# Kernel optimization log

Measured on AMD Instinct MI355X. Metric: run time of the kernel, lower is better.

Reference implementation:

```python
import jax, jax.numpy as jnp
import numpy as np
import math

N_HEADS = 8
INPUT_DIM = 128
EMBED_DIM = 128
KEY_DIM = EMBED_DIM // N_HEADS  # 16, val_dim == key_dim
B = 4
N = 1024


def setup_inputs() -> dict:
    key = jax.random.key(0)
    ks = jax.random.split(key, 12)
    def unif(k, shape):
        stdv = 1.0 / math.sqrt(shape[-1])
        return jax.random.uniform(k, shape, jnp.float32, -stdv, stdv)
    return {
        "q": jax.random.normal(ks[0], (B, N, INPUT_DIM), jnp.float32),
        "out_source_attn": jax.random.normal(ks[1], (N_HEADS, B, N, N), jnp.float32),
        "st_edge": jax.random.normal(ks[2], (N_HEADS, B, N, N), jnp.float32),
        "W_query": unif(ks[3], (N_HEADS, INPUT_DIM, KEY_DIM)),
        "W_key": unif(ks[4], (N_HEADS, INPUT_DIM, KEY_DIM)),
        "W_val": unif(ks[5], (N_HEADS, INPUT_DIM, KEY_DIM)),
        "w1": unif(ks[6], (8, 16)),  # Linear(16, 8) weight
        "b1": unif(ks[7], (8,)),
        "w2": unif(ks[8], (8, 8)),   # Linear(8, 8) weight
        "b2": unif(ks[9], (8,)),
        "W_out": unif(ks[10], (N_HEADS, KEY_DIM, EMBED_DIM)),
    }


def reference(q, out_source_attn, st_edge, W_query, W_key, W_val, w1, b1, w2, b2, W_out):
    norm = 1.0 / math.sqrt(KEY_DIM)
    # per-head projections: (h, B, N, k)
    Q = jnp.einsum('bni,hik->hbnk', q, W_query)
    K = jnp.einsum('bni,hik->hbnk', q, W_key)
    V = jnp.einsum('bni,hiv->hbnv', q, W_val)
    # compatibility scores + spatio-temporal edge bias, scaled
    compat = (jnp.einsum('hbnk,hbmk->hbnm', Q, K) + st_edge) * norm
    # concat on head axis -> (16, B, N, N)
    scores = jnp.concatenate([compat, out_source_attn], axis=0)
    # tiny per-position MLP over the 16 concatenated channels
    x = scores.transpose(1, 2, 3, 0)                 # (B, N, N, 16)
    x = jax.nn.relu(x @ w1.T + b1)                   # (B, N, N, 8)
    x = x @ w2.T + b2                                # (B, N, N, 8)
    attn_logits = x.transpose(3, 0, 1, 2)            # (8, B, N, N)
    attn = jax.nn.softmax(attn_logits, axis=-1)
    heads = jnp.einsum('hbnm,hbmv->hbnv', attn, V)   # (8, B, N, v)
    out = jnp.einsum('hbnv,hve->bne', heads, W_out)  # (B, N, embed)
    return (out, out_source_attn, st_edge)
```

## Files before the change

kernel.cpp:

```cpp
#include <hip/hip_runtime.h>

typedef _Float16 half_t;
typedef _Float16 half2_t __attribute__((ext_vector_type(2)));
typedef float f4 __attribute__((ext_vector_type(4)));

#define BB 4
#define NN 1024
#define NH 8
#define KD 16
#define ID 128
#define NT 4
#define LGR 520

static constexpr size_t OUT_SZ   = (size_t)BB * NN * 128;
static constexpr size_t ATT_SZ   = (size_t)NH * BB * NN * NN;
static constexpr size_t OFF_OSS  = OUT_SZ;
static constexpr size_t OFF_ST   = OUT_SZ + ATT_SZ;
static constexpr size_t HSTRIDE  = (size_t)BB * NN * NN;

__device__ __forceinline__ float fdot2u(unsigned int a, unsigned int b, float c) {
    union { unsigned int u; half2_t h; } ua, ub;
    ua.u = a; ub.u = b;
    return __builtin_amdgcn_fdot2(ua.h, ub.h, c, false);
}

__global__ __launch_bounds__(128) void qkv_kernel(
    const float* __restrict__ q,  const float* __restrict__ Wq,
    const float* __restrict__ Wk, const float* __restrict__ Wv,
    half_t* __restrict__ Qh, half_t* __restrict__ Kp, half_t* __restrict__ Vp)
{
    const int bn = blockIdx.x;
    const int j  = threadIdx.x;
    const int h  = j >> 4, k = j & 15;
    const int b  = bn >> 10, n = bn & 1023;

    __shared__ float qrow[ID];
    qrow[j] = q[(size_t)bn * ID + j];
    __syncthreads();

    const float* wq = Wq + h * ID * KD + k;
    const float* wk = Wk + h * ID * KD + k;
    const float* wv = Wv + h * ID * KD + k;
    float aq = 0.f, ak = 0.f, av = 0.f;
#pragma unroll
    for (int i = 0; i < ID; ++i) {
        float x = qrow[i];
        aq = fmaf(x, wq[i * KD], aq);
        ak = fmaf(x, wk[i * KD], ak);
        av = fmaf(x, wv[i * KD], av);
    }
    Qh[(size_t)bn * 128 + j] = (half_t)aq;
    const size_t pr = ((size_t)((b * NH + h) * 8 + (k >> 1)) * NN + n) * 2 + (k & 1);
    Kp[pr] = (half_t)ak;
    Vp[pr] = (half_t)av;
}

__global__ __launch_bounds__(256) void vtrans_kernel(
    const unsigned int* __restrict__ Vp, half_t* __restrict__ Vt)
{
    const int bh  = blockIdx.x >> 2;
    const int nt  = blockIdx.x & 3;
    const int tid = threadIdx.x;
    const int n0  = nt * 256;

    __shared__ half_t t[16][264];

#pragma unroll
    for (int vp = 0; vp < 8; ++vp) {
        union { unsigned int u; half_t h2[2]; } c;
        c.u = Vp[((size_t)(bh * 8 + vp)) * NN + n0 + tid];
        t[2 * vp + 0][tid] = c.h2[0];
        t[2 * vp + 1][tid] = c.h2[1];
    }
    __syncthreads();
#pragma unroll
    for (int rep = 0; rep < 2; ++rep) {
        const int cch = tid + rep * 256;
        const int row = cch >> 5, col = (cch & 31) * 8;
        const uint4 vv = *reinterpret_cast<const uint4*>(&t[row][col]);
        *reinterpret_cast<uint4*>(Vt + ((size_t)(bh * 16 + row)) * NN + n0 + col) = vv;
    }
}

__global__ __launch_bounds__(512, 4) void fused_kernel(
    const float* __restrict__ oss, const float* __restrict__ st,
    const half_t* __restrict__ Qh, const unsigned int* __restrict__ Kp,
    const half_t* __restrict__ Vt,
    const float* __restrict__ w1,  const float* __restrict__ b1,
    const float* __restrict__ w2,  const float* __restrict__ b2,
    const float* __restrict__ Wout, float* __restrict__ out)
{
    const int n0  = blockIdx.x * NT;
    const int b   = blockIdx.y;
    const int tid = threadIdx.x;
    const int rg  = tid >> 7;
    const int t7  = tid & 127;
    const int mi0 = t7 * 4;

    __shared__ __align__(16) unsigned int kst[8 * 512];
    __shared__ __align__(16) half_t lg[NT * NH * LGR];
    __shared__ unsigned int qsh[NT][64];
    __shared__ float wsumPart[8][NH];
    __shared__ float headsSh[NT][128];

    if (tid < 256) qsh[tid >> 6][tid & 63] =
        reinterpret_cast<const unsigned int*>(Qh + ((size_t)(b * NN + n0 + (tid >> 6))) * 128)[tid & 63];
    if (tid < 64) wsumPart[tid >> 3][tid & 7] = 0.f;
    __syncthreads();

    const int ph   = tid >> 6;
    const int pv   = (tid >> 2) & 15;
    const int psub = tid & 3;

    float pvAcc[NT] = {0.f, 0.f, 0.f, 0.f};

#pragma unroll 1
    for (int hf = 0; hf < 2; ++hf) {
        float y[4][8];
#pragma unroll
        for (int mo = 0; mo < 4; ++mo)
#pragma unroll
            for (int o = 0; o < 8; ++o) y[mo][o] = b1[o];

#pragma unroll 1
        for (int h = 0; h < NH; ++h) {
            __syncthreads();
            {
                const int kp = tid >> 6, c = (tid & 63) * 8;
                const unsigned int* src =
                    Kp + ((size_t)((b * NH + h) * 8 + kp)) * NN + hf * 512 + c;
                const uint4 A  = *reinterpret_cast<const uint4*>(src);
                const uint4 B2 = *reinterpret_cast<const uint4*>(src + 4);
                *reinterpret_cast<uint4*>(&kst[kp * 512 + c])     = A;
                *reinterpret_cast<uint4*>(&kst[kp * 512 + c + 4]) = B2;
            }
            __syncthreads();

            const size_t idx = (size_t)h * HSTRIDE +
                ((size_t)(b * NN + n0 + rg)) * NN + hf * 512 + mi0;
            const f4 sv = __builtin_nontemporal_load(reinterpret_cast<const f4*>(st + idx));
            const f4 ov = __builtin_nontemporal_load(reinterpret_cast<const f4*>(oss + idx));
            *reinterpret_cast<f4*>(out + OFF_ST + idx)  = sv;
            *reinterpret_cast<f4*>(out + OFF_OSS + idx) = ov;
            const float svv[4] = {sv.x, sv.y, sv.z, sv.w};
            const float ovv[4] = {ov.x, ov.y, ov.z, ov.w};

            float acc[4] = {0.f, 0.f, 0.f, 0.f};
#pragma unroll
            for (int kp = 0; kp < 8; ++kp) {
                const uint4 k4 = *reinterpret_cast<const uint4*>(&kst[kp * 512 + mi0]);
                const unsigned int qp = qsh[rg][h * 8 + kp];
                acc[0] = fdot2u(k4.x, qp, acc[0]);
                acc[1] = fdot2u(k4.y, qp, acc[1]);
                acc[2] = fdot2u(k4.z, qp, acc[2]);
                acc[3] = fdot2u(k4.w, qp, acc[3]);
            }

            float w1c[8], w1o[8];
#pragma unroll
            for (int o = 0; o < 8; ++o) { w1c[o] = w1[o * 16 + h]; w1o[o] = w1[o * 16 + 8 + h]; }
#pragma unroll
            for (int mo = 0; mo < 4; ++mo) {
                const float c = (acc[mo] + svv[mo]) * 0.25f;
#pragma unroll
                for (int o = 0; o < 8; ++o)
                    y[mo][o] = fmaf(c, w1c[o], fmaf(ovv[mo], w1o[o], y[mo][o]));
            }
        }

        float lgv[8][4];
#pragma unroll
        for (int mo = 0; mo < 4; ++mo) {
            float z[8];
#pragma unroll
            for (int o = 0; o < 8; ++o) z[o] = fmaxf(y[mo][o], 0.f);
#pragma unroll
            for (int p = 0; p < 8; ++p) {
                float a = b2[p];
#pragma unroll
                for (int o = 0; o < 8; ++o) a = fmaf(z[o], w2[p * 8 + o], a);
                lgv[p][mo] = a;
            }
        }
        float psum[8];
#pragma unroll
        for (int p = 0; p < 8; ++p) {
            const float e0 = __expf(lgv[p][0]);
            const float e1 = __expf(lgv[p][1]);
            const float e2 = __expf(lgv[p][2]);
            const float e3 = __expf(lgv[p][3]);
            psum[p] = (e0 + e1) + (e2 + e3);
            union { uint2 u; half_t h4[4]; } w;
            w.h4[0] = (half_t)e0; w.h4[1] = (half_t)e1;
            w.h4[2] = (half_t)e2; w.h4[3] = (half_t)e3;
            *reinterpret_cast<uint2*>(&lg[(rg * NH + p) * LGR + mi0]) = w.u;
        }
#pragma unroll
        for (int p = 0; p < 8; ++p)
#pragma unroll
            for (int s = 32; s > 0; s >>= 1)
                psum[p] += __shfl_xor(psum[p], s);
        if ((tid & 63) == 0) {
            const int w = tid >> 6;
#pragma unroll
            for (int p = 0; p < 8; ++p) wsumPart[w][p] += psum[p];
        }
        __syncthreads();

        {
            const unsigned int* vr = reinterpret_cast<const unsigned int*>(
                Vt + ((size_t)((b * NH + ph) * KD + pv)) * NN + hf * 512);
#pragma unroll 2
            for (int c2 = 0; c2 < 16; ++c2) {
                const int mo = (c2 * 4 + psub) * 8;
                const uint4 vv = *reinterpret_cast<const uint4*>(vr + mo / 2);
#pragma unroll
                for (int r = 0; r < NT; ++r) {
                    const uint4 ww = *reinterpret_cast<const uint4*>(&lg[(r * NH + ph) * LGR + mo]);
                    pvAcc[r] = fdot2u(vv.x, ww.x, pvAcc[r]);
                    pvAcc[r] = fdot2u(vv.y, ww.y, pvAcc[r]);
                    pvAcc[r] = fdot2u(vv.z, ww.z, pvAcc[r]);
                    pvAcc[r] = fdot2u(vv.w, ww.w, pvAcc[r]);
                }
            }
        }
        __syncthreads();
    }

#pragma unroll
    for (int r = 0; r < NT; ++r) {
        pvAcc[r] += __shfl_xor(pvAcc[r], 1);
        pvAcc[r] += __shfl_xor(pvAcc[r], 2);
    }
    if (psub == 0) {
#pragma unroll
        for (int r = 0; r < NT; ++r) {
            const float s = wsumPart[2 * r][ph] + wsumPart[2 * r + 1][ph];
            headsSh[r][ph * 16 + pv] = pvAcc[r] * (1.0f / s);
        }
    }
    __syncthreads();

    {
        const int e  = tid & 127;
        const int q2 = tid >> 7;
        float a[NT] = {0.f, 0.f, 0.f, 0.f};
#pragma unroll
        for (int ii = 0; ii < 32; ++ii) {
            const int i = q2 * 32 + ii;
            const float wr = Wout[(size_t)i * 128 + e];
#pragma unroll
            for (int r = 0; r < NT; ++r) a[r] = fmaf(headsSh[r][i], wr, a[r]);
        }
        float* red = reinterpret_cast<float*>(kst);
#pragma unroll
        for (int r = 0; r < NT; ++r) red[(q2 * NT + r) * 128 + e] = a[r];
        __syncthreads();
        {
            const int r = tid >> 7, e2 = tid & 127;
            out[((size_t)(b * NN + n0 + r)) * 128 + e2] =
                red[(0 * NT + r) * 128 + e2] + red[(1 * NT + r) * 128 + e2] +
                red[(2 * NT + r) * 128 + e2] + red[(3 * NT + r) * 128 + e2];
        }
    }
}

extern "C" void kernel_launch(void* const* d_in, const int* in_sizes, int n_in,
                              void* d_out, int out_size, void* d_ws, size_t ws_size,
                              hipStream_t stream) {
    const float* q    = (const float*)d_in[0];
    const float* oss  = (const float*)d_in[1];
    const float* st   = (const float*)d_in[2];
    const float* Wq   = (const float*)d_in[3];
    const float* Wk   = (const float*)d_in[4];
    const float* Wv   = (const float*)d_in[5];
    const float* w1   = (const float*)d_in[6];
    const float* b1   = (const float*)d_in[7];
    const float* w2   = (const float*)d_in[8];
    const float* b2   = (const float*)d_in[9];
    const float* Wout = (const float*)d_in[10];
    float* out = (float*)d_out;

    half_t* Qh = (half_t*)d_ws;
    half_t* Kp = (half_t*)((char*)d_ws + 1u * 1024u * 1024u);
    half_t* Vp = (half_t*)((char*)d_ws + 2u * 1024u * 1024u);
    half_t* Vt = (half_t*)((char*)d_ws + 3u * 1024u * 1024u);

    qkv_kernel<<<dim3(BB * NN), dim3(128), 0, stream>>>(q, Wq, Wk, Wv, Qh, Kp, Vp);
    vtrans_kernel<<<dim3(32 * 4), dim3(256), 0, stream>>>((const unsigned int*)Vp, Vt);
    fused_kernel<<<dim3(NN / NT, BB), dim3(512), 0, stream>>>(
        oss, st, Qh, (const unsigned int*)Kp, Vt,
        w1, b1, w2, b2, Wout, out);
}
```

Before: 156.5 us.

## Process eight query rows per block with 256-wide key tiles

Each block now handles eight query rows instead of four, and the key dimension is split into four tiles of 256 instead of two of 512. One wavefront now owns a whole row, so the per-row softmax sum no longer needs to combine partial sums from two waves. This halves the number of blocks and doubles the reuse of each staged K tile and V row across query rows, with the goal of cutting redundant K/V traffic. The occupancy hint rises to 6 blocks per SM to go with the smaller shared-memory footprint, at the cost of twice as many tile iterations with their barriers.

```diff
diff --git a/kernel.cpp b/kernel.cpp
--- a/kernel.cpp
+++ b/kernel.cpp
@@ -9,8 +9,9 @@
 #define NH 8
 #define KD 16
 #define ID 128
-#define NT 4
-#define LGR 520
+#define NT 8
+#define QM 256
+#define LGR 264
 
 static constexpr size_t OUT_SZ   = (size_t)BB * NN * 128;
 static constexpr size_t ATT_SZ   = (size_t)NH * BB * NN * NN;
@@ -82,7 +83,7 @@
     }
 }
 
-__global__ __launch_bounds__(512, 4) void fused_kernel(
+__global__ __launch_bounds__(512, 6) void fused_kernel(
     const float* __restrict__ oss, const float* __restrict__ st,
     const half_t* __restrict__ Qh, const unsigned int* __restrict__ Kp,
     const half_t* __restrict__ Vt,
@@ -93,29 +94,29 @@
     const int n0  = blockIdx.x * NT;
     const int b   = blockIdx.y;
     const int tid = threadIdx.x;
-    const int rg  = tid >> 7;
-    const int t7  = tid & 127;
-    const int mi0 = t7 * 4;
-
-    __shared__ __align__(16) unsigned int kst[8 * 512];
+    const int rg  = tid >> 6;
+    const int t6  = tid & 63;
+    const int mi0 = t6 * 4;
+
+    __shared__ __align__(16) unsigned int kst[8 * QM];
     __shared__ __align__(16) half_t lg[NT * NH * LGR];
     __shared__ unsigned int qsh[NT][64];
-    __shared__ float wsumPart[8][NH];
+    __shared__ float wsum[NT][NH];
     __shared__ float headsSh[NT][128];
 
-    if (tid < 256) qsh[tid >> 6][tid & 63] =
-        reinterpret_cast<const unsigned int*>(Qh + ((size_t)(b * NN + n0 + (tid >> 6))) * 128)[tid & 63];
-    if (tid < 64) wsumPart[tid >> 3][tid & 7] = 0.f;
+    qsh[tid >> 6][tid & 63] = reinterpret_cast<const unsigned int*>(
+        Qh + ((size_t)(b * NN + n0 + (tid >> 6))) * 128)[tid & 63];
+    if (tid < 64) wsum[tid >> 3][tid & 7] = 0.f;
     __syncthreads();
 
     const int ph   = tid >> 6;
     const int pv   = (tid >> 2) & 15;
     const int psub = tid & 3;
 
-    float pvAcc[NT] = {0.f, 0.f, 0.f, 0.f};
+    float pvAcc[NT] = {0.f, 0.f, 0.f, 0.f, 0.f, 0.f, 0.f, 0.f};
 
 #pragma unroll 1
-    for (int hf = 0; hf < 2; ++hf) {
+    for (int qt = 0; qt < 4; ++qt) {
         float y[4][8];
 #pragma unroll
         for (int mo = 0; mo < 4; ++mo)
@@ -126,18 +127,16 @@
         for (int h = 0; h < NH; ++h) {
             __syncthreads();
             {
-                const int kp = tid >> 6, c = (tid & 63) * 8;
+                const int kp = tid >> 6, c = (tid & 63) * 4;
                 const unsigned int* src =
-                    Kp + ((size_t)((b * NH + h) * 8 + kp)) * NN + hf * 512 + c;
-                const uint4 A  = *reinterpret_cast<const uint4*>(src);
-                const uint4 B2 = *reinterpret_cast<const uint4*>(src + 4);
-                *reinterpret_cast<uint4*>(&kst[kp * 512 + c])     = A;
-                *reinterpret_cast<uint4*>(&kst[kp * 512 + c + 4]) = B2;
+                    Kp + ((size_t)((b * NH + h) * 8 + kp)) * NN + qt * QM + c;
+                *reinterpret_cast<uint4*>(&kst[kp * QM + c]) =
+                    *reinterpret_cast<const uint4*>(src);
             }
             __syncthreads();
 
             const size_t idx = (size_t)h * HSTRIDE +
-                ((size_t)(b * NN + n0 + rg)) * NN + hf * 512 + mi0;
+                ((size_t)(b * NN + n0 + rg)) * NN + qt * QM + mi0;
             const f4 sv = __builtin_nontemporal_load(reinterpret_cast<const f4*>(st + idx));
             const f4 ov = __builtin_nontemporal_load(reinterpret_cast<const f4*>(oss + idx));
             *reinterpret_cast<f4*>(out + OFF_ST + idx)  = sv;
@@ -148,7 +147,7 @@
             float acc[4] = {0.f, 0.f, 0.f, 0.f};
 #pragma unroll
             for (int kp = 0; kp < 8; ++kp) {
-                const uint4 k4 = *reinterpret_cast<const uint4*>(&kst[kp * 512 + mi0]);
+                const uint4 k4 = *reinterpret_cast<const uint4*>(&kst[kp * QM + mi0]);
                 const unsigned int qp = qsh[rg][h * 8 + kp];
                 acc[0] = fdot2u(k4.x, qp, acc[0]);
                 acc[1] = fdot2u(k4.y, qp, acc[1]);
@@ -200,18 +199,17 @@
 #pragma unroll
             for (int s = 32; s > 0; s >>= 1)
                 psum[p] += __shfl_xor(psum[p], s);
-        if ((tid & 63) == 0) {
-            const int w = tid >> 6;
-#pragma unroll
-            for (int p = 0; p < 8; ++p) wsumPart[w][p] += psum[p];
+        if (t6 == 0) {
+#pragma unroll
+            for (int p = 0; p < 8; ++p) wsum[rg][p] += psum[p];
         }
         __syncthreads();
 
         {
             const unsigned int* vr = reinterpret_cast<const unsigned int*>(
-                Vt + ((size_t)((b * NH + ph) * KD + pv)) * NN + hf * 512);
+                Vt + ((size_t)((b * NH + ph) * KD + pv)) * NN + qt * QM);
 #pragma unroll 2
-            for (int c2 = 0; c2 < 16; ++c2) {
+            for (int c2 = 0; c2 < 8; ++c2) {
                 const int mo = (c2 * 4 + psub) * 8;
                 const uint4 vv = *reinterpret_cast<const uint4*>(vr + mo / 2);
 #pragma unroll
@@ -234,17 +232,15 @@
     }
     if (psub == 0) {
 #pragma unroll
-        for (int r = 0; r < NT; ++r) {
-            const float s = wsumPart[2 * r][ph] + wsumPart[2 * r + 1][ph];
-            headsSh[r][ph * 16 + pv] = pvAcc[r] * (1.0f / s);
-        }
+        for (int r = 0; r < NT; ++r)
+            headsSh[r][ph * 16 + pv] = pvAcc[r] * (1.0f / wsum[r][ph]);
     }
     __syncthreads();
 
     {
         const int e  = tid & 127;
         const int q2 = tid >> 7;
-        float a[NT] = {0.f, 0.f, 0.f, 0.f};
+        float a[NT] = {0.f, 0.f, 0.f, 0.f, 0.f, 0.f, 0.f, 0.f};
 #pragma unroll
         for (int ii = 0; ii < 32; ++ii) {
             const int i = q2 * 32 + ii;
@@ -252,15 +248,17 @@
 #pragma unroll
             for (int r = 0; r < NT; ++r) a[r] = fmaf(headsSh[r][i], wr, a[r]);
         }
-        float* red = reinterpret_cast<float*>(kst);
+        float* red = reinterpret_cast<float*>(lg);
 #pragma unroll
         for (int r = 0; r < NT; ++r) red[(q2 * NT + r) * 128 + e] = a[r];
         __syncthreads();
-        {
-            const int r = tid >> 7, e2 = tid & 127;
+#pragma unroll
+        for (int rep = 0; rep < 2; ++rep) {
+            const int idx = rep * 512 + tid;
+            const int r = idx >> 7, e2 = idx & 127;
             out[((size_t)(b * NN + n0 + r)) * 128 + e2] =
-                red[(0 * NT + r) * 128 + e2] + red[(1 * NT + r) * 128 + e2] +
-                red[(2 * NT + r) * 128 + e2] + red[(3 * NT + r) * 128 + e2];
+                (red[(0 * NT + r) * 128 + e2] + red[(1 * NT + r) * 128 + e2]) +
+                (red[(2 * NT + r) * 128 + e2] + red[(3 * NT + r) * 128 + e2]);
         }
     }
 }
```

Result: slower. 203.4 us (+29.9%).

## Prefetch next head's K tile and edge inputs into registers across head loop

Applied to the files above, without the earlier changes.

Software-pipelines the per-head loop: the K tile and the st/oss float4 loads for head h+1 are issued into registers while head h is being computed, and the K registers are then written to shared memory at the top of the next iteration. This hides global-load latency behind the dot-product and MLP work. The launch bounds are also raised from 4 to 6 blocks per CU, which caps register use and could cause spills, especially now that the prefetch keeps more values live.

```diff
diff --git a/kernel.cpp b/kernel.cpp
--- a/kernel.cpp
+++ b/kernel.cpp
@@ -82,7 +82,7 @@
     }
 }
 
-__global__ __launch_bounds__(512, 4) void fused_kernel(
+__global__ __launch_bounds__(512, 6) void fused_kernel(
     const float* __restrict__ oss, const float* __restrict__ st,
     const half_t* __restrict__ Qh, const unsigned int* __restrict__ Kp,
     const half_t* __restrict__ Vt,
@@ -114,6 +114,8 @@
 
     float pvAcc[NT] = {0.f, 0.f, 0.f, 0.f};
 
+    const int kp = tid >> 6, kc = (tid & 63) * 8;
+
 #pragma unroll 1
     for (int hf = 0; hf < 2; ++hf) {
         float y[4][8];
@@ -122,24 +124,36 @@
 #pragma unroll
             for (int o = 0; o < 8; ++o) y[mo][o] = b1[o];
 
+        const unsigned int* kSrc0 =
+            Kp + ((size_t)((b * NH + 0) * 8 + kp)) * NN + hf * 512 + kc;
+        uint4 kA = *reinterpret_cast<const uint4*>(kSrc0);
+        uint4 kB = *reinterpret_cast<const uint4*>(kSrc0 + 4);
+        const size_t rowOff = ((size_t)(b * NN + n0 + rg)) * NN + hf * 512 + mi0;
+        f4 sv_c = __builtin_nontemporal_load(reinterpret_cast<const f4*>(st + rowOff));
+        f4 ov_c = __builtin_nontemporal_load(reinterpret_cast<const f4*>(oss + rowOff));
+
 #pragma unroll 1
         for (int h = 0; h < NH; ++h) {
             __syncthreads();
-            {
-                const int kp = tid >> 6, c = (tid & 63) * 8;
-                const unsigned int* src =
-                    Kp + ((size_t)((b * NH + h) * 8 + kp)) * NN + hf * 512 + c;
-                const uint4 A  = *reinterpret_cast<const uint4*>(src);
-                const uint4 B2 = *reinterpret_cast<const uint4*>(src + 4);
-                *reinterpret_cast<uint4*>(&kst[kp * 512 + c])     = A;
-                *reinterpret_cast<uint4*>(&kst[kp * 512 + c + 4]) = B2;
-            }
+            *reinterpret_cast<uint4*>(&kst[kp * 512 + kc])     = kA;
+            *reinterpret_cast<uint4*>(&kst[kp * 512 + kc + 4]) = kB;
             __syncthreads();
 
-            const size_t idx = (size_t)h * HSTRIDE +
-                ((size_t)(b * NN + n0 + rg)) * NN + hf * 512 + mi0;
-            const f4 sv = __builtin_nontemporal_load(reinterpret_cast<const f4*>(st + idx));
-            const f4 ov = __builtin_nontemporal_load(reinterpret_cast<const f4*>(oss + idx));
+            const size_t idx = (size_t)h * HSTRIDE + rowOff;
+
+            if (h < 7) {
+                const unsigned int* kSrcN =
+                    Kp + ((size_t)((b * NH + h + 1) * 8 + kp)) * NN + hf * 512 + kc;
+                kA = *reinterpret_cast<const uint4*>(kSrcN);
+                kB = *reinterpret_cast<const uint4*>(kSrcN + 4);
+            }
+            const f4 sv = sv_c, ov = ov_c;
+            if (h < 7) {
+                const size_t idxN = idx + HSTRIDE;
+                sv_c = __builtin_nontemporal_load(reinterpret_cast<const f4*>(st + idxN));
+                ov_c = __builtin_nontemporal_load(reinterpret_cast<const f4*>(oss + idxN));
+            }
+
             *reinterpret_cast<f4*>(out + OFF_ST + idx)  = sv;
             *reinterpret_cast<f4*>(out + OFF_OSS + idx) = ov;
             const float svv[4] = {sv.x, sv.y, sv.z, sv.w};
@@ -147,9 +161,9 @@
 
             float acc[4] = {0.f, 0.f, 0.f, 0.f};
 #pragma unroll
-            for (int kp = 0; kp < 8; ++kp) {
-                const uint4 k4 = *reinterpret_cast<const uint4*>(&kst[kp * 512 + mi0]);
-                const unsigned int qp = qsh[rg][h * 8 + kp];
+            for (int kp2 = 0; kp2 < 8; ++kp2) {
+                const uint4 k4 = *reinterpret_cast<const uint4*>(&kst[kp2 * 512 + mi0]);
+                const unsigned int qp = qsh[rg][h * 8 + kp2];
                 acc[0] = fdot2u(k4.x, qp, acc[0]);
                 acc[1] = fdot2u(k4.y, qp, acc[1]);
                 acc[2] = fdot2u(k4.z, qp, acc[2]);
```

After: 248.3 us. +58.6%, slower.
